# Optimization experiments

Hardware: AMD Instinct MI355X
Metric: run time of the kernel (lower is better)

Reference implementation:

```python
import jax, jax.numpy as jnp
import numpy as np

B, L, E, H = 4, 2048, 512, 8
HD = E // H
EPS = 1e-6


def setup_inputs() -> dict:
    key = jax.random.key(0)
    ks = jax.random.split(key, 9)
    s = 0.02
    return {
        "query": jax.random.normal(ks[0], (B, L, E), dtype=jnp.float32),
        "Wq": jax.random.normal(ks[1], (E, E), dtype=jnp.float32) * s,
        "bq": jnp.zeros((E,), dtype=jnp.float32),
        "Wk": jax.random.normal(ks[2], (E, E), dtype=jnp.float32) * s,
        "bk": jnp.zeros((E,), dtype=jnp.float32),
        "Wv": jax.random.normal(ks[3], (E, E), dtype=jnp.float32) * s,
        "bv": jnp.zeros((E,), dtype=jnp.float32),
        "Wo": jax.random.normal(ks[4], (E, E), dtype=jnp.float32) * s,
        "bo": jnp.zeros((E,), dtype=jnp.float32),
    }


def reference(query, Wq, bq, Wk, bk, Wv, bv, Wo, bo):
    b, tgt_len, embed_dim = query.shape
    n_head = H
    head_dim = embed_dim // n_head
    # Faithful to the source: a raw view (reshape), NOT a transpose.
    x = query.reshape(tgt_len, b, embed_dim)  # (L, B, E)
    q = x @ Wq.T + bq
    k = x @ Wk.T + bk
    v = x @ Wv.T + bv
    # softmax over head_dim, per head
    q = jax.nn.softmax(q.reshape(tgt_len, b, n_head, head_dim), axis=-1)
    k = jax.nn.softmax(k.reshape(tgt_len, b, n_head, head_dim), axis=-1)
    # (L, B*H, hd) -> (B*H, L, hd)
    q_ = q.reshape(tgt_len, b * n_head, head_dim).swapaxes(0, 1)
    k_ = k.reshape(tgt_len, b * n_head, head_dim).swapaxes(0, 1)
    comp_q_ = 1.0 - q_
    comp_k_ = 1.0 - k_
    v_ = v.reshape(tgt_len, b * n_head, head_dim).swapaxes(0, 1)
    # non-causal XNor attention: scores from q.k^T + (1-q).(1-k)^T
    weights = jnp.einsum('nld,nsd->nls', q_, k_) + jnp.einsum('nld,nsd->nls', comp_q_, comp_k_)
    denom = jnp.clip(jnp.sum(weights, axis=-1, keepdims=True), EPS, None)
    attn_weights = weights / denom
    attn_output = jnp.einsum('nls,nsd->nld', attn_weights, v_)  # (B*H, L, hd)
    attn_output = attn_output.swapaxes(0, 1).reshape(tgt_len, b, embed_dim)
    out = attn_output @ Wo.T + bo
    return out.reshape(b, tgt_len, embed_dim)
```

## Files before the change

kernel.cpp:

```cpp
#include <hip/hip_runtime.h>

#define B_ 4
#define L_ 2048
#define E_ 512
#define H_ 8
#define NROW (B_*L_)
#define SZ (NROW*E_)
#define NH (B_*H_)

typedef unsigned short u16;
typedef unsigned int u32;
typedef __attribute__((ext_vector_type(8))) __bf16 bf16x8;
typedef __attribute__((ext_vector_type(8))) u16 u16x8;
typedef __attribute__((ext_vector_type(4))) float f32x4;

__device__ __forceinline__ u16 f2bf(float f) {
  union { float f; u32 u; } v; v.f = f;
  u32 r = v.u + 0x7FFFu + ((v.u >> 16) & 1u);
  return (u16)(r >> 16);
}
__device__ __forceinline__ float bf2f(u16 s) {
  union { u32 u; float f; } v; v.u = ((u32)s) << 16;
  return v.f;
}
__device__ __forceinline__ void async16(const u16* g, u16* l) {
  __builtin_amdgcn_global_load_lds(
      (const __attribute__((address_space(1))) u32*)g,
      (__attribute__((address_space(3))) u32*)l, 16, 0, 0);
}

__global__ __launch_bounds__(256) void cvt_all(const float* __restrict__ X,
    const float* __restrict__ W0, const float* __restrict__ W1,
    const float* __restrict__ W2, const float* __restrict__ W3,
    u16* __restrict__ Y, u16* __restrict__ Y0, u16* __restrict__ Y1,
    u16* __restrict__ Y2, u16* __restrict__ Y3) {
  const int bid = blockIdx.x;
  const float* src;
  u16* dst;
  int off;
  if (bid < 2048) { src = X; dst = Y; off = bid * 2048; }
  else {
    const int t = bid - 2048, s = t >> 7, r = t & 127;
    src = (s == 0) ? W0 : (s == 1) ? W1 : (s == 2) ? W2 : W3;
    dst = (s == 0) ? Y0 : (s == 1) ? Y1 : (s == 2) ? Y2 : Y3;
    off = r * 2048;
  }
  const int i0 = off + threadIdx.x * 8;
  f32x4 a = *(const f32x4*)(src + i0);
  f32x4 b = *(const f32x4*)(src + i0 + 4);
  u16x8 o;
#pragma unroll
  for (int j = 0; j < 4; ++j) { o[j] = f2bf(a[j]); o[4 + j] = f2bf(b[j]); }
  *(u16x8*)(dst + i0) = o;
}

__global__ __launch_bounds__(256) void qkv_gemm(const u16* __restrict__ X,
    const u16* __restrict__ Wq, const u16* __restrict__ Wk, const u16* __restrict__ Wv,
    const float* __restrict__ bq, const float* __restrict__ bk, const float* __restrict__ bv,
    u16* __restrict__ Qo, u16* __restrict__ Ko, u16* __restrict__ Vo) {
  __shared__ __align__(16) u16 sA[128 * 32];
  __shared__ __align__(16) u16 sB[128 * 32];
  const int z = blockIdx.z;
  const u16* W = (z == 0) ? Wq : (z == 1) ? Wk : Wv;
  const float* bias = (z == 0) ? bq : (z == 1) ? bk : bv;
  u16* C = (z == 0) ? Qo : (z == 1) ? Ko : Vo;
  const int tid = threadIdx.x;
  const int w = tid >> 6, lane = tid & 63;
  const int bm = blockIdx.x * 128, bn = blockIdx.y * 128;
  const int wm = (w >> 1) * 64, wn = (w & 1) * 64;
  const int lrow = lane >> 2, lk = (lane & 3) * 8;
  const int fr = lane & 15, quad = lane >> 4;
  f32x4 acc[4][4] = {};
  for (int k0 = 0; k0 < E_; k0 += 32) {
    __syncthreads();
#pragma unroll
    for (int j = 0; j < 2; ++j) {
      const int rb = j * 64 + w * 16;
      async16(X + (size_t)(bm + rb + lrow) * E_ + k0 + lk, sA + rb * 32);
      async16(W + (size_t)(bn + rb + lrow) * E_ + k0 + lk, sB + rb * 32);
    }
    __syncthreads();
    bf16x8 af[4], bfr[4];
#pragma unroll
    for (int t = 0; t < 4; ++t) {
      af[t]  = *(const bf16x8*)(sA + (wm + t * 16 + fr) * 32 + quad * 8);
      bfr[t] = *(const bf16x8*)(sB + (wn + t * 16 + fr) * 32 + quad * 8);
    }
#pragma unroll
    for (int i = 0; i < 4; ++i)
#pragma unroll
      for (int j = 0; j < 4; ++j)
        acc[i][j] = __builtin_amdgcn_mfma_f32_16x16x32_bf16(af[i], bfr[j], acc[i][j], 0, 0, 0);
  }
  if (z < 2) {
#pragma unroll
    for (int i = 0; i < 4; ++i)
#pragma unroll
      for (int r = 0; r < 4; ++r) {
        float v[4];
#pragma unroll
        for (int j = 0; j < 4; ++j)
          v[j] = acc[i][j][r] + bias[bn + wn + j * 16 + fr];
        float mx = fmaxf(fmaxf(v[0], v[1]), fmaxf(v[2], v[3]));
#pragma unroll
        for (int off = 1; off < 16; off <<= 1) mx = fmaxf(mx, __shfl_xor(mx, off, 64));
        float e[4], s = 0.f;
#pragma unroll
        for (int j = 0; j < 4; ++j) { e[j] = __expf(v[j] - mx); s += e[j]; }
#pragma unroll
        for (int off = 1; off < 16; off <<= 1) s += __shfl_xor(s, off, 64);
        const float inv = 1.f / s;
        const int row = bm + wm + i * 16 + quad * 4 + r;
#pragma unroll
        for (int j = 0; j < 4; ++j)
          C[(size_t)row * E_ + bn + wn + j * 16 + fr] = f2bf(e[j] * inv);
      }
  } else {
#pragma unroll
    for (int i = 0; i < 4; ++i)
#pragma unroll
      for (int r = 0; r < 4; ++r) {
        const int row = bm + wm + i * 16 + quad * 4 + r;
#pragma unroll
        for (int j = 0; j < 4; ++j) {
          const int col = bn + wn + j * 16 + fr;
          C[(size_t)row * E_ + col] = f2bf(acc[i][j][r] + bias[col]);
        }
      }
  }
}

__global__ __launch_bounds__(256) void gemm_out(const u16* __restrict__ X,
    const u16* __restrict__ W, const float* __restrict__ bias, float* __restrict__ C) {
  __shared__ __align__(16) u16 sA[128 * 32];
  __shared__ __align__(16) u16 sB[128 * 32];
  const int tid = threadIdx.x;
  const int w = tid >> 6, lane = tid & 63;
  const int bm = blockIdx.x * 128, bn = blockIdx.y * 128;
  const int wm = (w >> 1) * 64, wn = (w & 1) * 64;
  const int lrow = lane >> 2, lk = (lane & 3) * 8;
  const int fr = lane & 15, quad = lane >> 4;
  f32x4 acc[4][4] = {};
  for (int k0 = 0; k0 < E_; k0 += 32) {
    __syncthreads();
#pragma unroll
    for (int j = 0; j < 2; ++j) {
      const int rb = j * 64 + w * 16;
      async16(X + (size_t)(bm + rb + lrow) * E_ + k0 + lk, sA + rb * 32);
      async16(W + (size_t)(bn + rb + lrow) * E_ + k0 + lk, sB + rb * 32);
    }
    __syncthreads();
    bf16x8 af[4], bfr[4];
#pragma unroll
    for (int t = 0; t < 4; ++t) {
      af[t]  = *(const bf16x8*)(sA + (wm + t * 16 + fr) * 32 + quad * 8);
      bfr[t] = *(const bf16x8*)(sB + (wn + t * 16 + fr) * 32 + quad * 8);
    }
#pragma unroll
    for (int i = 0; i < 4; ++i)
#pragma unroll
      for (int j = 0; j < 4; ++j)
        acc[i][j] = __builtin_amdgcn_mfma_f32_16x16x32_bf16(af[i], bfr[j], acc[i][j], 0, 0, 0);
  }
#pragma unroll
  for (int i = 0; i < 4; ++i)
#pragma unroll
    for (int r = 0; r < 4; ++r) {
      const int row = bm + wm + i * 16 + quad * 4 + r;
#pragma unroll
      for (int j = 0; j < 4; ++j) {
        const int col = bn + wn + j * 16 + fr;
        C[(size_t)row * E_ + col] = acc[i][j][r] + bias[col];
      }
    }
}

__global__ __launch_bounds__(256) void kv_part(const u16* __restrict__ K,
    const u16* __restrict__ V, float* __restrict__ Part,
    float* __restrict__ KPart, float* __restrict__ VPart) {
  const int n = blockIdx.x, b = n >> 3, h = n & 7;
  const int sy = blockIdx.y;
  const int tid = threadIdx.x;
  const int td = tid & 15, te = tid >> 4;
  __shared__ float sK[32][68], sV[32][68];
  float acc[4][4] = {};
  float srow = 0.f;
  const int which = tid >> 7, sub = tid & 127;
  const int lr = sub >> 2, ck = (sub & 3) * 16;
  const u16* src = which ? V : K;
  float* dstrow = which ? &sV[lr][ck] : &sK[lr][ck];
  const int l0beg = sy * 128;
  for (int l0 = l0beg; l0 < l0beg + 128; l0 += 32) {
    const u16* g = src + (size_t)((l0 + lr) * B_ + b) * E_ + h * 64 + ck;
    u16x8 d0 = *(const u16x8*)g;
    u16x8 d1 = *(const u16x8*)(g + 8);
    __syncthreads();
    f32x4 f0, f1, f2, f3;
#pragma unroll
    for (int j = 0; j < 4; ++j) {
      f0[j] = bf2f(d0[j]); f1[j] = bf2f(d0[4 + j]);
      f2[j] = bf2f(d1[j]); f3[j] = bf2f(d1[4 + j]);
    }
    *(f32x4*)(dstrow) = f0; *(f32x4*)(dstrow + 4) = f1;
    *(f32x4*)(dstrow + 8) = f2; *(f32x4*)(dstrow + 12) = f3;
    __syncthreads();
#pragma unroll 8
    for (int p = 0; p < 32; ++p) {
      f32x4 kk = *(const f32x4*)&sK[p][td * 4];
      f32x4 vv = *(const f32x4*)&sV[p][te * 4];
#pragma unroll
      for (int i = 0; i < 4; ++i)
#pragma unroll
        for (int j = 0; j < 4; ++j)
          acc[i][j] = fmaf(kk[i], vv[j], acc[i][j]);
      if (tid < 64) srow += sK[p][tid];
      else if (tid < 128) srow += sV[p][tid - 64];
    }
  }
  float* Pp = Part + (size_t)(n * 16 + sy) * 4096;
#pragma unroll
  for (int j = 0; j < 4; ++j) {
    f32x4 v4 = {acc[0][j], acc[1][j], acc[2][j], acc[3][j]};
    *(f32x4*)(Pp + (te * 4 + j) * 64 + td * 4) = v4;
  }
  if (tid < 64) KPart[(n * 16 + sy) * 64 + tid] = srow;
  else if (tid < 128) VPart[(n * 16 + sy) * 64 + tid - 64] = srow;
}

__global__ __launch_bounds__(256) void kv_merge(const float* __restrict__ Part,
    const float* __restrict__ KPart, const float* __restrict__ VPart,
    float* __restrict__ Mt, float* __restrict__ Ks, float* __restrict__ Vs) {
  const int bid = blockIdx.x, tid = threadIdx.x;
  if (bid < 512) {
    const int oi = bid * 256 + tid;
    const int n = oi >> 12, j = oi & 4095;
    const float* p = Part + (size_t)n * 16 * 4096 + j;
    float s = 0.f;
#pragma unroll
    for (int sl = 0; sl < 16; ++sl) s += p[sl * 4096];
    Mt[oi] = s;
  } else {
    const int i = (bid - 512) * 256 + tid;
    const int which = i >> 11, rem = i & 2047;
    const int n = rem >> 6, d = rem & 63;
    const float* p = (which ? VPart : KPart) + (n * 16) * 64 + d;
    float s = 0.f;
#pragma unroll
    for (int sl = 0; sl < 16; ++sl) s += p[sl * 64];
    if (which) Vs[n * 64 + d] = s; else Ks[n * 64 + d] = s;
  }
}

__global__ __launch_bounds__(256) void apply_mfma(const u16* __restrict__ Qbf,
    const float* __restrict__ Mt, const float* __restrict__ Ksum,
    const float* __restrict__ Vsum, u16* __restrict__ Abf) {
  __shared__ __align__(16) u16 sQ[128 * 64];
  __shared__ __align__(16) u16 sM[64 * 64];
  __shared__ float sKs[64], sVs[64], sDen[128];
  const int n = blockIdx.x, b = n >> 3, h = n & 7;
  const int l0 = blockIdx.y * 128;
  const int tid = threadIdx.x, w = tid >> 6, lane = tid & 63;
  const int fr = lane & 15, quad = lane >> 4;
#pragma unroll
  for (int j = 0; j < 4; ++j) {
    const int rloc = w * 32 + j * 8;
    const int row = rloc + (lane >> 3);
    const int k = (lane & 7) * 8;
    async16(Qbf + (size_t)((l0 + row) * B_ + b) * E_ + h * 64 + k, sQ + rloc * 64);
  }
  {
    const float* Mp = Mt + (size_t)n * 4096 + tid * 16;
    f32x4 m0 = *(const f32x4*)(Mp);
    f32x4 m1 = *(const f32x4*)(Mp + 4);
    f32x4 m2 = *(const f32x4*)(Mp + 8);
    f32x4 m3 = *(const f32x4*)(Mp + 12);
    u16x8 o0, o1;
#pragma unroll
    for (int j = 0; j < 4; ++j) {
      o0[j] = f2bf(m0[j]); o0[4 + j] = f2bf(m1[j]);
      o1[j] = f2bf(m2[j]); o1[4 + j] = f2bf(m3[j]);
    }
    *(u16x8*)(sM + tid * 16) = o0;
    *(u16x8*)(sM + tid * 16 + 8) = o1;
  }
  if (tid < 64) sKs[tid] = Ksum[n * 64 + tid];
  else if (tid < 128) sVs[tid - 64] = Vsum[n * 64 + tid - 64];
  __syncthreads();
  union { u16x8 u; bf16x8 bv; } aU[2][2];
  bf16x8 bF[4][2];
#pragma unroll
  for (int mt = 0; mt < 2; ++mt)
#pragma unroll
    for (int ks = 0; ks < 2; ++ks)
      aU[mt][ks].u = *(const u16x8*)(sQ + (w * 32 + mt * 16 + fr) * 64 + ks * 32 + quad * 8);
#pragma unroll
  for (int nt = 0; nt < 4; ++nt)
#pragma unroll
    for (int ks = 0; ks < 2; ++ks)
      bF[nt][ks] = *(const bf16x8*)(sM + (nt * 16 + fr) * 64 + ks * 32 + quad * 8);
  float pden[2] = {0.f, 0.f};
#pragma unroll
  for (int mt = 0; mt < 2; ++mt)
#pragma unroll
    for (int ks = 0; ks < 2; ++ks)
#pragma unroll
      for (int j = 0; j < 8; ++j)
        pden[mt] = fmaf(bf2f(aU[mt][ks].u[j]), sKs[ks * 32 + quad * 8 + j], pden[mt]);
#pragma unroll
  for (int mt = 0; mt < 2; ++mt) {
    pden[mt] += __shfl_xor(pden[mt], 16, 64);
    pden[mt] += __shfl_xor(pden[mt], 32, 64);
    if (quad == 0)
      sDen[w * 32 + mt * 16 + fr] = fmaxf(2.f * pden[mt] + 62.f * (float)L_, 1e-6f);
  }
  __syncthreads();
  f32x4 acc[2][4];
#pragma unroll
  for (int mt = 0; mt < 2; ++mt)
#pragma unroll
    for (int nt = 0; nt < 4; ++nt) {
      const float iv = 31.f * sVs[nt * 16 + fr];
      acc[mt][nt] = (f32x4){iv, iv, iv, iv};
#pragma unroll
      for (int ks = 0; ks < 2; ++ks)
        acc[mt][nt] = __builtin_amdgcn_mfma_f32_16x16x32_bf16(aU[mt][ks].bv, bF[nt][ks],
                                                              acc[mt][nt], 0, 0, 0);
    }
#pragma unroll
  for (int mt = 0; mt < 2; ++mt)
#pragma unroll
    for (int r = 0; r < 4; ++r) {
      const int rloc = w * 32 + mt * 16 + quad * 4 + r;
      const float invd = 2.f / sDen[rloc];
      const size_t orow = (size_t)((l0 + rloc) * B_ + b) * E_ + h * 64;
#pragma unroll
      for (int nt = 0; nt < 4; ++nt)
        Abf[orow + nt * 16 + fr] = f2bf(acc[mt][nt][r] * invd);
    }
}

extern "C" void kernel_launch(void* const* d_in, const int* in_sizes, int n_in,
                              void* d_out, int out_size, void* d_ws, size_t ws_size,
                              hipStream_t stream) {
  const float* query = (const float*)d_in[0];
  const float* Wq = (const float*)d_in[1];
  const float* bq = (const float*)d_in[2];
  const float* Wk = (const float*)d_in[3];
  const float* bk = (const float*)d_in[4];
  const float* Wv = (const float*)d_in[5];
  const float* bv = (const float*)d_in[6];
  const float* Wo = (const float*)d_in[7];
  const float* bo = (const float*)d_in[8];
  float* out = (float*)d_out;

  char* ws = (char*)d_ws;
  u16* Xbf  = (u16*)(ws);
  u16* Qbf  = (u16*)(ws + 8388608);
  u16* Kbf  = (u16*)(ws + 16777216);
  u16* Vbf  = (u16*)(ws + 25165824);
  u16* Abf  = (u16*)(ws + 33554432);
  u16* Wqb  = (u16*)(ws + 41943040);
  u16* Wkb  = (u16*)(ws + 42467328);
  u16* Wvb  = (u16*)(ws + 42991616);
  u16* Wob  = (u16*)(ws + 43515904);
  float* Mt = (float*)(ws + 44040192);
  float* Ks = (float*)(ws + 44564480);
  float* Vs = (float*)(ws + 44572672);
  float* KPart = (float*)(ws + 44580864);
  float* VPart = (float*)(ws + 44711936);
  float* Part  = (float*)Xbf;

  cvt_all<<<2560, 256, 0, stream>>>(query, Wq, Wk, Wv, Wo,
                                    Xbf, Wqb, Wkb, Wvb, Wob);
  qkv_gemm<<<dim3(NROW / 128, E_ / 128, 3), 256, 0, stream>>>(
      Xbf, Wqb, Wkb, Wvb, bq, bk, bv, Qbf, Kbf, Vbf);
  kv_part<<<dim3(NH, 16), 256, 0, stream>>>(Kbf, Vbf, Part, KPart, VPart);
  kv_merge<<<528, 256, 0, stream>>>(Part, KPart, VPart, Mt, Ks, Vs);
  apply_mfma<<<dim3(NH, L_ / 128), 256, 0, stream>>>(Qbf, Mt, Ks, Vs, Abf);
  gemm_out<<<dim3(NROW / 128, E_ / 128), 256, 0, stream>>>(Abf, Wob, bo, out);
}
```

Before: 151.9 us.

## Use 128x64 GEMM tiles and stage epilogue through LDS for coalesced stores

```diff
diff --git a/kernel.cpp b/kernel.cpp
--- a/kernel.cpp
+++ b/kernel.cpp
@@ -58,121 +58,127 @@
     const u16* __restrict__ Wq, const u16* __restrict__ Wk, const u16* __restrict__ Wv,
     const float* __restrict__ bq, const float* __restrict__ bk, const float* __restrict__ bv,
     u16* __restrict__ Qo, u16* __restrict__ Ko, u16* __restrict__ Vo) {
-  __shared__ __align__(16) u16 sA[128 * 32];
-  __shared__ __align__(16) u16 sB[128 * 32];
+  __shared__ __align__(16) union {
+    struct { u16 a[128 * 32]; u16 b[64 * 32]; } st;
+    u16 ep[4][16 * 72];
+  } sh;
   const int z = blockIdx.z;
   const u16* W = (z == 0) ? Wq : (z == 1) ? Wk : Wv;
   const float* bias = (z == 0) ? bq : (z == 1) ? bk : bv;
   u16* C = (z == 0) ? Qo : (z == 1) ? Ko : Vo;
   const int tid = threadIdx.x;
   const int w = tid >> 6, lane = tid & 63;
-  const int bm = blockIdx.x * 128, bn = blockIdx.y * 128;
-  const int wm = (w >> 1) * 64, wn = (w & 1) * 64;
-  const int lrow = lane >> 2, lk = (lane & 3) * 8;
+  const int bm = blockIdx.x * 128, bn = blockIdx.y * 64;
   const int fr = lane & 15, quad = lane >> 4;
-  f32x4 acc[4][4] = {};
+  const int c0 = tid, c1 = tid + 256;
+  f32x4 acc[2][4] = {};
   for (int k0 = 0; k0 < E_; k0 += 32) {
     __syncthreads();
-#pragma unroll
-    for (int j = 0; j < 2; ++j) {
-      const int rb = j * 64 + w * 16;
-      async16(X + (size_t)(bm + rb + lrow) * E_ + k0 + lk, sA + rb * 32);
-      async16(W + (size_t)(bn + rb + lrow) * E_ + k0 + lk, sB + rb * 32);
-    }
-    __syncthreads();
-    bf16x8 af[4], bfr[4];
-#pragma unroll
-    for (int t = 0; t < 4; ++t) {
-      af[t]  = *(const bf16x8*)(sA + (wm + t * 16 + fr) * 32 + quad * 8);
-      bfr[t] = *(const bf16x8*)(sB + (wn + t * 16 + fr) * 32 + quad * 8);
-    }
-#pragma unroll
-    for (int i = 0; i < 4; ++i)
-#pragma unroll
-      for (int j = 0; j < 4; ++j)
-        acc[i][j] = __builtin_amdgcn_mfma_f32_16x16x32_bf16(af[i], bfr[j], acc[i][j], 0, 0, 0);
-  }
-  if (z < 2) {
-#pragma unroll
-    for (int i = 0; i < 4; ++i)
+    async16(X + (size_t)(bm + (c0 >> 2)) * E_ + k0 + (c0 & 3) * 8, sh.st.a + c0 * 8);
+    async16(X + (size_t)(bm + (c1 >> 2)) * E_ + k0 + (c1 & 3) * 8, sh.st.a + c1 * 8);
+    async16(W + (size_t)(bn + (c0 >> 2)) * E_ + k0 + (c0 & 3) * 8, sh.st.b + c0 * 8);
+    __syncthreads();
+    bf16x8 af[2], bf[4];
+#pragma unroll
+    for (int mt = 0; mt < 2; ++mt)
+      af[mt] = *(const bf16x8*)(sh.st.a + (w * 32 + mt * 16 + fr) * 32 + quad * 8);
+#pragma unroll
+    for (int nt = 0; nt < 4; ++nt)
+      bf[nt] = *(const bf16x8*)(sh.st.b + (nt * 16 + fr) * 32 + quad * 8);
+#pragma unroll
+    for (int mt = 0; mt < 2; ++mt)
+#pragma unroll
+      for (int nt = 0; nt < 4; ++nt)
+        acc[mt][nt] = __builtin_amdgcn_mfma_f32_16x16x32_bf16(af[mt], bf[nt], acc[mt][nt], 0, 0, 0);
+  }
+  __syncthreads();
+  u16* ep = sh.ep[w];
+#pragma unroll
+  for (int mt = 0; mt < 2; ++mt) {
+    if (z < 2) {
 #pragma unroll
       for (int r = 0; r < 4; ++r) {
         float v[4];
 #pragma unroll
-        for (int j = 0; j < 4; ++j)
-          v[j] = acc[i][j][r] + bias[bn + wn + j * 16 + fr];
+        for (int nt = 0; nt < 4; ++nt)
+          v[nt] = acc[mt][nt][r] + bias[bn + nt * 16 + fr];
         float mx = fmaxf(fmaxf(v[0], v[1]), fmaxf(v[2], v[3]));
 #pragma unroll
         for (int off = 1; off < 16; off <<= 1) mx = fmaxf(mx, __shfl_xor(mx, off, 64));
-        float e[4], s = 0.f;
-#pragma unroll
-        for (int j = 0; j < 4; ++j) { e[j] = __expf(v[j] - mx); s += e[j]; }
-#pragma unroll
-        for (int off = 1; off < 16; off <<= 1) s += __shfl_xor(s, off, 64);
-        const float inv = 1.f / s;
-        const int row = bm + wm + i * 16 + quad * 4 + r;
-#pragma unroll
-        for (int j = 0; j < 4; ++j)
-          C[(size_t)row * E_ + bn + wn + j * 16 + fr] = f2bf(e[j] * inv);
+        float e[4], ssum = 0.f;
+#pragma unroll
+        for (int nt = 0; nt < 4; ++nt) { e[nt] = __expf(v[nt] - mx); ssum += e[nt]; }
+#pragma unroll
+        for (int off = 1; off < 16; off <<= 1) ssum += __shfl_xor(ssum, off, 64);
+        const float inv = 1.f / ssum;
+#pragma unroll
+        for (int nt = 0; nt < 4; ++nt)
+          ep[(quad * 4 + r) * 72 + nt * 16 + fr] = f2bf(e[nt] * inv);
       }
-  } else {
-#pragma unroll
-    for (int i = 0; i < 4; ++i)
-#pragma unroll
-      for (int r = 0; r < 4; ++r) {
-        const int row = bm + wm + i * 16 + quad * 4 + r;
-#pragma unroll
-        for (int j = 0; j < 4; ++j) {
-          const int col = bn + wn + j * 16 + fr;
-          C[(size_t)row * E_ + col] = f2bf(acc[i][j][r] + bias[col]);
-        }
-      }
+    } else {
+#pragma unroll
+      for (int r = 0; r < 4; ++r)
+#pragma unroll
+        for (int nt = 0; nt < 4; ++nt)
+          ep[(quad * 4 + r) * 72 + nt * 16 + fr] = f2bf(acc[mt][nt][r] + bias[bn + nt * 16 + fr]);
+    }
+#pragma unroll
+    for (int pass = 0; pass < 2; ++pass) {
+      const int row = pass * 8 + (lane >> 3), ch = lane & 7;
+      u16x8 val = *(const u16x8*)(ep + row * 72 + ch * 8);
+      *(u16x8*)(C + (size_t)(bm + w * 32 + mt * 16 + row) * E_ + bn + ch * 8) = val;
+    }
   }
 }
 
 __global__ __launch_bounds__(256) void gemm_out(const u16* __restrict__ X,
     const u16* __restrict__ W, const float* __restrict__ bias, float* __restrict__ C) {
-  __shared__ __align__(16) u16 sA[128 * 32];
-  __shared__ __align__(16) u16 sB[128 * 32];
+  __shared__ __align__(16) union {
+    struct { u16 a[128 * 32]; u16 b[64 * 32]; } st;
+    float ep[4][16 * 68];
+  } sh;
   const int tid = threadIdx.x;
   const int w = tid >> 6, lane = tid & 63;
-  const int bm = blockIdx.x * 128, bn = blockIdx.y * 128;
-  const int wm = (w >> 1) * 64, wn = (w & 1) * 64;
-  const int lrow = lane >> 2, lk = (lane & 3) * 8;
+  const int bm = blockIdx.x * 128, bn = blockIdx.y * 64;
   const int fr = lane & 15, quad = lane >> 4;
-  f32x4 acc[4][4] = {};
+  const int c0 = tid, c1 = tid + 256;
+  f32x4 acc[2][4] = {};
   for (int k0 = 0; k0 < E_; k0 += 32) {
     __syncthreads();
-#pragma unroll
-    for (int j = 0; j < 2; ++j) {
-      const int rb = j * 64 + w * 16;
-      async16(X + (size_t)(bm + rb + lrow) * E_ + k0 + lk, sA + rb * 32);
-      async16(W + (size_t)(bn + rb + lrow) * E_ + k0 + lk, sB + rb * 32);
-    }
-    __syncthreads();
-    bf16x8 af[4], bfr[4];
-#pragma unroll
-    for (int t = 0; t < 4; ++t) {
-      af[t]  = *(const bf16x8*)(sA + (wm + t * 16 + fr) * 32 + quad * 8);
-      bfr[t] = *(const bf16x8*)(sB + (wn + t * 16 + fr) * 32 + quad * 8);
-    }
-#pragma unroll
-    for (int i = 0; i < 4; ++i)
-#pragma unroll
-      for (int j = 0; j < 4; ++j)
-        acc[i][j] = __builtin_amdgcn_mfma_f32_16x16x32_bf16(af[i], bfr[j], acc[i][j], 0, 0, 0);
-  }
-#pragma unroll
-  for (int i = 0; i < 4; ++i)
-#pragma unroll
-    for (int r = 0; r < 4; ++r) {
-      const int row = bm + wm + i * 16 + quad * 4 + r;
-#pragma unroll
-      for (int j = 0; j < 4; ++j) {
-        const int col = bn + wn + j * 16 + fr;
-        C[(size_t)row * E_ + col] = acc[i][j][r] + bias[col];
-      }
-    }
+    async16(X + (size_t)(bm + (c0 >> 2)) * E_ + k0 + (c0 & 3) * 8, sh.st.a + c0 * 8);
+    async16(X + (size_t)(bm + (c1 >> 2)) * E_ + k0 + (c1 & 3) * 8, sh.st.a + c1 * 8);
+    async16(W + (size_t)(bn + (c0 >> 2)) * E_ + k0 + (c0 & 3) * 8, sh.st.b + c0 * 8);
+    __syncthreads();
+    bf16x8 af[2], bf[4];
+#pragma unroll
+    for (int mt = 0; mt < 2; ++mt)
+      af[mt] = *(const bf16x8*)(sh.st.a + (w * 32 + mt * 16 + fr) * 32 + quad * 8);
+#pragma unroll
+    for (int nt = 0; nt < 4; ++nt)
+      bf[nt] = *(const bf16x8*)(sh.st.b + (nt * 16 + fr) * 32 + quad * 8);
+#pragma unroll
+    for (int mt = 0; mt < 2; ++mt)
+#pragma unroll
+      for (int nt = 0; nt < 4; ++nt)
+        acc[mt][nt] = __builtin_amdgcn_mfma_f32_16x16x32_bf16(af[mt], bf[nt], acc[mt][nt], 0, 0, 0);
+  }
+  __syncthreads();
+  float* ep = sh.ep[w];
+#pragma unroll
+  for (int mt = 0; mt < 2; ++mt) {
+#pragma unroll
+    for (int r = 0; r < 4; ++r)
+#pragma unroll
+      for (int nt = 0; nt < 4; ++nt)
+        ep[(quad * 4 + r) * 68 + nt * 16 + fr] = acc[mt][nt][r] + bias[bn + nt * 16 + fr];
+#pragma unroll
+    for (int p = 0; p < 4; ++p) {
+      const int id = p * 64 + lane;
+      const int row = id >> 4, ch = id & 15;
+      f32x4 val = *(const f32x4*)(ep + row * 68 + ch * 4);
+      *(f32x4*)(C + (size_t)(bm + w * 32 + mt * 16 + row) * E_ + bn + ch * 4) = val;
+    }
+  }
 }
 
 __global__ __launch_bounds__(256) void kv_part(const u16* __restrict__ K,
@@ -372,10 +378,10 @@
 
   cvt_all<<<2560, 256, 0, stream>>>(query, Wq, Wk, Wv, Wo,
                                     Xbf, Wqb, Wkb, Wvb, Wob);
-  qkv_gemm<<<dim3(NROW / 128, E_ / 128, 3), 256, 0, stream>>>(
+  qkv_gemm<<<dim3(NROW / 128, E_ / 64, 3), 256, 0, stream>>>(
       Xbf, Wqb, Wkb, Wvb, bq, bk, bv, Qbf, Kbf, Vbf);
   kv_part<<<dim3(NH, 16), 256, 0, stream>>>(Kbf, Vbf, Part, KPart, VPart);
   kv_merge<<<528, 256, 0, stream>>>(Part, KPart, VPart, Mt, Ks, Vs);
   apply_mfma<<<dim3(NH, L_ / 128), 256, 0, stream>>>(Qbf, Mt, Ks, Vs, Abf);
-  gemm_out<<<dim3(NROW / 128, E_ / 128), 256, 0, stream>>>(Abf, Wob, bo, out);
-}
+  gemm_out<<<dim3(NROW / 128, E_ / 64), 256, 0, stream>>>(Abf, Wob, bo, out);
+}
```

Result: faster. 146.7 us (-3.4%).
